# Performance work log

Measured on AMD Instinct MI355X. Metric: run time of the kernel, lower is better.

Reference implementation:

```python
import jax, jax.numpy as jnp
import numpy as np

D_MODEL, N_HEAD, D_FF = 768, 12, 3072
HEAD_DIM = D_MODEL // N_HEAD
EPS = 1e-5


def _layernorm(x, g, b):
    mu = jnp.mean(x, axis=-1, keepdims=True)
    var = jnp.mean((x - mu) ** 2, axis=-1, keepdims=True)
    return (x - mu) * jax.lax.rsqrt(var + EPS) * g + b


def setup_inputs() -> dict:
    key = jax.random.key(0)
    ks = jax.random.split(key, 14)
    s = 1.0 / np.sqrt(D_MODEL)
    sf = 1.0 / np.sqrt(D_FF)
    inp = {
        "x": jax.random.normal(ks[0], (2, 2048, D_MODEL), dtype=jnp.float32),
        "Wq": jax.random.normal(ks[1], (D_MODEL, D_MODEL), dtype=jnp.float32) * s,
        "bq": jnp.zeros((D_MODEL,), jnp.float32),
        "Wk": jax.random.normal(ks[2], (D_MODEL, D_MODEL), dtype=jnp.float32) * s,
        "bk": jnp.zeros((D_MODEL,), jnp.float32),
        "Wv": jax.random.normal(ks[3], (D_MODEL, D_MODEL), dtype=jnp.float32) * s,
        "bv": jnp.zeros((D_MODEL,), jnp.float32),
        "Wo": jax.random.normal(ks[4], (D_MODEL, D_MODEL), dtype=jnp.float32) * s,
        "bo": jnp.zeros((D_MODEL,), jnp.float32),
        "W1": jax.random.normal(ks[5], (D_MODEL, D_FF), dtype=jnp.float32) * s,
        "b1": jnp.zeros((D_FF,), jnp.float32),
        "W2": jax.random.normal(ks[6], (D_FF, D_MODEL), dtype=jnp.float32) * sf,
        "b2": jnp.zeros((D_MODEL,), jnp.float32),
        "ln1_g": jnp.ones((D_MODEL,), jnp.float32),
        "ln1_b": jnp.zeros((D_MODEL,), jnp.float32),
        "ln2_g": jnp.ones((D_MODEL,), jnp.float32),
        "ln2_b": jnp.zeros((D_MODEL,), jnp.float32),
    }
    return inp


def reference(x, Wq, bq, Wk, bk, Wv, bv, Wo, bo, W1, b1, W2, b2,
              ln1_g, ln1_b, ln2_g, ln2_b):
    B, S, D = x.shape
    # projections -> [B, H, S, hd]
    def proj(W, b):
        return (x @ W + b).reshape(B, S, N_HEAD, HEAD_DIM).transpose(0, 2, 1, 3)
    q, k, v = proj(Wq, bq), proj(Wk, bk), proj(Wv, bv)
    scores = jnp.einsum("bhqd,bhkd->bhqk", q, k) / jnp.sqrt(
        jnp.asarray(HEAD_DIM, jnp.float32))
    attn = jax.nn.softmax(scores, axis=-1)
    ctx = jnp.einsum("bhqk,bhkd->bhqd", attn, v)
    ctx = ctx.transpose(0, 2, 1, 3).reshape(B, S, D)
    attn_out = ctx @ Wo + bo
    h = _layernorm(x + attn_out, ln1_g, ln1_b)
    ffn = jax.nn.gelu(h @ W1 + b1, approximate=False) @ W2 + b2
    return _layernorm(h + ffn, ln2_g, ln2_b)
```

## Files before the change

kernel.cpp:

```cpp
#include <hip/hip_runtime.h>
#include <hip/hip_bf16.h>
#include <cstdint>
#include <cstddef>

typedef unsigned short u16;
typedef __bf16 bf16x8 __attribute__((ext_vector_type(8)));
typedef float f32x4 __attribute__((ext_vector_type(4)));

#define MFMA_BF16(a, b, c) __builtin_amdgcn_mfma_f32_16x16x32_bf16((a), (b), (c), 0, 0, 0)

#define GLDS16(g, l)                                                        \
  __builtin_amdgcn_global_load_lds(                                         \
      (__attribute__((address_space(1))) void*)(void*)(g),                  \
      (__attribute__((address_space(3))) void*)(void*)(l), 16, 0, 0)

#define QSCALE 0.18033688011112042f
#define PSTRIDE ((size_t)4096 * 768)

__device__ __forceinline__ u16 f2bf(float x) {
  union { float f; unsigned u; } c; c.f = x;
  unsigned u = c.u;
  unsigned r = (u + 0x7fffu + ((u >> 16) & 1u)) >> 16;
  return (u16)r;
}


__global__ __launch_bounds__(256) void transpose_bf16_k(
    const float* __restrict__ in, u16* __restrict__ out, int K, int N) {
  __shared__ float tile[32][33];
  const int tx = threadIdx.x & 31, ty = threadIdx.x >> 5;
  const int bx = blockIdx.x * 32;
  const int by = blockIdx.y * 32;
#pragma unroll
  for (int j = 0; j < 32; j += 8)
    tile[ty + j][tx] = in[(size_t)(by + ty + j) * N + bx + tx];
  __syncthreads();
#pragma unroll
  for (int j = 0; j < 32; j += 8)
    out[(size_t)(bx + ty + j) * K + by + tx] = f2bf(tile[tx][ty + j]);
}

__global__ __launch_bounds__(256) void cvt_bf16_k(
    const float* __restrict__ in, u16* __restrict__ out, int n) {
  int i = (blockIdx.x * 256 + threadIdx.x) * 4;
  if (i + 3 < n) {
    const float4 v = *(const float4*)(in + i);
    ushort4 o;
    o.x = f2bf(v.x); o.y = f2bf(v.y); o.z = f2bf(v.z); o.w = f2bf(v.w);
    *(ushort4*)(out + i) = o;
  }
}

__global__ __launch_bounds__(256) void concat3_k(
    const float* __restrict__ a, const float* __restrict__ b,
    const float* __restrict__ c, float* __restrict__ out) {
  int i = blockIdx.x * 256 + threadIdx.x;
  if (i < 768) out[i] = a[i];
  else if (i < 1536) out[i] = b[i - 768];
  else if (i < 2304) out[i] = c[i - 1536];
}

template <int EPI>
__global__ __launch_bounds__(256) void gemm_bt(
    const u16* __restrict__ A, const u16* __restrict__ BT,
    const float* __restrict__ bias, int M, int N, int K, int kchunk,
    float* __restrict__ outf, u16* __restrict__ outb,
    u16* __restrict__ qo, u16* __restrict__ ko, u16* __restrict__ vto) {
  __shared__ __align__(16) u16 lsA[128 * 64];
  __shared__ __align__(16) u16 lsB[128 * 64];
  const int tid = threadIdx.x;
  const int w = tid >> 6, lane = tid & 63;
  const int wm = w & 1, wn = w >> 1;
  const int lrow = lane & 15, quad = lane >> 4;
  const int m0 = blockIdx.y * 128, n0 = blockIdx.x * 128;
  const int kbeg = blockIdx.z * kchunk, kend = kbeg + kchunk;

  f32x4 acc[4][4];
#pragma unroll
  for (int i = 0; i < 4; ++i)
#pragma unroll
    for (int j = 0; j < 4; ++j) acc[i][j] = (f32x4){0.f, 0.f, 0.f, 0.f};

  const int off = tid * 16;
  const int srow = off >> 7;
  const int schunk = (off >> 4) & 7;
  const int sxc = schunk ^ (srow & 7);
  const int scol = sxc * 8;

  const int rsw = lrow & 7;

  for (int k0 = kbeg; k0 < kend; k0 += 64) {
    const u16* ga = A + (size_t)(m0 + srow) * K + k0 + scol;
    const u16* gb = BT + (size_t)(n0 + srow) * K + k0 + scol;
#pragma unroll
    for (int c = 0; c < 4; ++c) {
      GLDS16(ga + (size_t)(c * 32) * K, (char*)lsA + c * 4096 + off);
      GLDS16(gb + (size_t)(c * 32) * K, (char*)lsB + c * 4096 + off);
    }
    __syncthreads();
#pragma unroll
    for (int ks = 0; ks < 2; ++ks) {
      const int slot = ((ks * 4 + quad) ^ rsw) * 8;
      bf16x8 af[4], bfr[4];
#pragma unroll
      for (int ms = 0; ms < 4; ++ms)
        af[ms] = *(const bf16x8*)&lsA[(wm * 64 + ms * 16 + lrow) * 64 + slot];
#pragma unroll
      for (int ns = 0; ns < 4; ++ns)
        bfr[ns] = *(const bf16x8*)&lsB[(wn * 64 + ns * 16 + lrow) * 64 + slot];
#pragma unroll
      for (int ms = 0; ms < 4; ++ms)
#pragma unroll
        for (int ns = 0; ns < 4; ++ns)
          acc[ms][ns] = MFMA_BF16(af[ms], bfr[ns], acc[ms][ns]);
    }
    __syncthreads();
  }

  float* const pf = (EPI == 3) ? outf + (size_t)blockIdx.z * M * N : outf;
#pragma unroll
  for (int ms = 0; ms < 4; ++ms) {
    const int rbase = m0 + wm * 64 + ms * 16 + quad * 4;
#pragma unroll
    for (int ns = 0; ns < 4; ++ns) {
      const int col = n0 + wn * 64 + ns * 16 + lrow;
      if constexpr (EPI == 3) {
#pragma unroll
        for (int r = 0; r < 4; ++r)
          pf[(size_t)(rbase + r) * N + col] = acc[ms][ns][r];
      } else if constexpr (EPI == 2) {
        const float bcol = bias[col];
#pragma unroll
        for (int r = 0; r < 4; ++r) {
          float v = acc[ms][ns][r] + bcol;
          float g = 0.5f * v * (1.0f + erff(v * 0.7071067811865476f));
          outb[(size_t)(rbase + r) * N + col] = f2bf(g);
        }
      } else {
        const float bcol = bias[col];
        const int which = col / 768;
        const int rem = col - which * 768;
        const int hh = rem >> 6, dd = rem & 63;
        const int bI = rbase >> 11, sI = rbase & 2047;
        const size_t bh = (size_t)bI * 12 + hh;
        if (which == 0) {
#pragma unroll
          for (int r = 0; r < 4; ++r)
            qo[(bh * 2048 + sI + r) * 64 + dd] = f2bf((acc[ms][ns][r] + bcol) * QSCALE);
        } else if (which == 1) {
#pragma unroll
          for (int r = 0; r < 4; ++r)
            ko[(bh * 2048 + sI + r) * 64 + dd] = f2bf(acc[ms][ns][r] + bcol);
        } else {
          ushort4 pk;
          pk.x = f2bf(acc[ms][ns][0] + bcol);
          pk.y = f2bf(acc[ms][ns][1] + bcol);
          pk.z = f2bf(acc[ms][ns][2] + bcol);
          pk.w = f2bf(acc[ms][ns][3] + bcol);
          *(ushort4*)(vto + (bh * 64 + dd) * 2048 + sI) = pk;
        }
      }
    }
  }
}

__global__ __launch_bounds__(256) void attn_kernel(
    const u16* __restrict__ q, const u16* __restrict__ k,
    const u16* __restrict__ vT, u16* __restrict__ ctx) {
  __shared__ __align__(16) u16 lsK[64 * 64];
  __shared__ __align__(16) u16 lsV[64 * 64];
  __shared__ __align__(16) u16 lsP[4][16 * 64];
  const int tid = threadIdx.x;
  const int w = tid >> 6, lane = tid & 63;
  const int lrow = lane & 15, quad = lane >> 4;
  const int bh = blockIdx.y;
  const int b = bh / 12, h = bh - b * 12;
  const int q0 = blockIdx.x * 64;

  const u16* qbase = q + (size_t)bh * 2048 * 64;
  const u16* kbase = k + (size_t)bh * 2048 * 64;
  const u16* vbase = vT + (size_t)bh * 64 * 2048;

  const int qrow = q0 + w * 16 + lrow;
  const bf16x8 qf0 = *(const bf16x8*)(qbase + (size_t)qrow * 64 + quad * 8);
  const bf16x8 qf1 = *(const bf16x8*)(qbase + (size_t)qrow * 64 + 32 + quad * 8);

  float lsum[4] = {0.f, 0.f, 0.f, 0.f};
  f32x4 oacc[4];
#pragma unroll
  for (int d = 0; d < 4; ++d) oacc[d] = (f32x4){0.f, 0.f, 0.f, 0.f};

  const int off = tid * 16;
  const int srow = off >> 7;
  const int schunk = (off >> 4) & 7;
  const int sxc = schunk ^ (srow & 7);
  const int ksrc = srow * 64 + sxc * 8;
  const int vsrc0 = srow * 2048 + sxc * 8;

  const int c0 = quad ^ (lrow & 7);
  const int rd0 = c0 * 8, rd1 = (c0 ^ 4) * 8;

  u16* const lsPw = &lsP[w][0];
  const int jhi_base = lrow >> 3, jlo = lrow & 7;

  for (int kt = 0; kt < 2048; kt += 64) {
    GLDS16(kbase + (size_t)kt * 64 + ksrc, (char*)lsK + off);
    GLDS16(kbase + (size_t)(kt + 32) * 64 + ksrc, (char*)lsK + 4096 + off);
    GLDS16(vbase + vsrc0 + kt, (char*)lsV + off);
    GLDS16(vbase + vsrc0 + kt + 32 * 2048, (char*)lsV + 4096 + off);
    __syncthreads();

    f32x4 sc[4];
#pragma unroll
    for (int ns = 0; ns < 4; ++ns) {
      sc[ns] = (f32x4){0.f, 0.f, 0.f, 0.f};
      const u16* kr = &lsK[(ns * 16 + lrow) * 64];
      bf16x8 kf0 = *(const bf16x8*)(kr + rd0);
      bf16x8 kf1 = *(const bf16x8*)(kr + rd1);
      sc[ns] = MFMA_BF16(qf0, kf0, sc[ns]);
      sc[ns] = MFMA_BF16(qf1, kf1, sc[ns]);
    }

#pragma unroll
    for (int ns = 0; ns < 4; ++ns) {
      const int jhi = ns * 2 + jhi_base;
#pragma unroll
      for (int r = 0; r < 4; ++r) {
        float p = __builtin_amdgcn_exp2f(sc[ns][r]);
        lsum[r] += p;
        union { float f; unsigned u; } cv; cv.f = p;
        const int m = quad * 4 + r;
        lsPw[m * 64 + ((jhi ^ (m & 7)) * 8) + jlo] = (u16)(cv.u >> 16);
      }
    }

    const u16* pr = lsPw + lrow * 64;
    const bf16x8 pf0 = *(const bf16x8*)(pr + rd0);
    const bf16x8 pf1 = *(const bf16x8*)(pr + rd1);
#pragma unroll
    for (int d = 0; d < 4; ++d) {
      const u16* vr = &lsV[(d * 16 + lrow) * 64];
      bf16x8 vf0 = *(const bf16x8*)(vr + rd0);
      bf16x8 vf1 = *(const bf16x8*)(vr + rd1);
      oacc[d] = MFMA_BF16(pf0, vf0, oacc[d]);
      oacc[d] = MFMA_BF16(pf1, vf1, oacc[d]);
    }
    __syncthreads();
  }

#pragma unroll
  for (int r = 0; r < 4; ++r) {
#pragma unroll
    for (int mm = 1; mm <= 8; mm <<= 1) lsum[r] += __shfl_xor(lsum[r], mm);
  }
  float invl[4];
#pragma unroll
  for (int r = 0; r < 4; ++r) invl[r] = 1.f / lsum[r];

  const int srow_out = q0 + w * 16 + quad * 4;
#pragma unroll
  for (int d = 0; d < 4; ++d)
#pragma unroll
    for (int r = 0; r < 4; ++r)
      ctx[(size_t)(b * 2048 + srow_out + r) * 768 + h * 64 + d * 16 + lrow] =
          f2bf(oacc[d][r] * invl[r]);
}

__global__ __launch_bounds__(256) void ln_kernel(
    const float* __restrict__ parts, int nparts, const float* __restrict__ bias,
    const float* __restrict__ res, const float* __restrict__ g,
    const float* __restrict__ bb, float* __restrict__ outf, u16* __restrict__ outb) {
  const int row = blockIdx.x;
  const int tid = threadIdx.x;
  const float* pr = res + (size_t)row * 768;
  float v[3], s = 0.f, s2 = 0.f;
#pragma unroll
  for (int j = 0; j < 3; ++j) {
    const int c = tid + j * 256;
    float t = bias[c] + pr[c];
    for (int p = 0; p < nparts; ++p)
      t += parts[p * PSTRIDE + (size_t)row * 768 + c];
    v[j] = t; s += t; s2 += t * t;
  }
#pragma unroll
  for (int m = 32; m > 0; m >>= 1) {
    s += __shfl_xor(s, m);
    s2 += __shfl_xor(s2, m);
  }
  __shared__ float red[8];
  const int w = tid >> 6, lane = tid & 63;
  if (lane == 0) { red[w] = s; red[4 + w] = s2; }
  __syncthreads();
  s = red[0] + red[1] + red[2] + red[3];
  s2 = red[4] + red[5] + red[6] + red[7];
  const float mu = s * (1.f / 768.f);
  const float var = s2 * (1.f / 768.f) - mu * mu;
  const float rstd = rsqrtf(var + 1e-5f);
#pragma unroll
  for (int j = 0; j < 3; ++j) {
    const int c = tid + j * 256;
    const float y = (v[j] - mu) * rstd * g[c] + bb[c];
    if (outf) outf[(size_t)row * 768 + c] = y;
    if (outb) outb[(size_t)row * 768 + c] = f2bf(y);
  }
}

extern "C" void kernel_launch(void* const* d_in, const int* in_sizes, int n_in,
                              void* d_out, int out_size, void* d_ws, size_t ws_size,
                              hipStream_t stream) {
  const float* x    = (const float*)d_in[0];
  const float* Wq   = (const float*)d_in[1];
  const float* bq   = (const float*)d_in[2];
  const float* Wk   = (const float*)d_in[3];
  const float* bk   = (const float*)d_in[4];
  const float* Wv   = (const float*)d_in[5];
  const float* bv   = (const float*)d_in[6];
  const float* Wo   = (const float*)d_in[7];
  const float* bo   = (const float*)d_in[8];
  const float* W1   = (const float*)d_in[9];
  const float* b1   = (const float*)d_in[10];
  const float* W2   = (const float*)d_in[11];
  const float* b2   = (const float*)d_in[12];
  const float* ln1g = (const float*)d_in[13];
  const float* ln1b = (const float*)d_in[14];
  const float* ln2g = (const float*)d_in[15];
  const float* ln2b = (const float*)d_in[16];

  char* ws = (char*)d_ws;
  size_t off = 0;
  auto alloc = [&](size_t bytes) {
    void* p = ws + off;
    off += (bytes + 255) & ~(size_t)255;
    return p;
  };
  u16*  WqkvT = (u16*)alloc(2304ull * 768 * 2);
  u16*  WoT   = (u16*)alloc(768ull * 768 * 2);
  u16*  W1T   = (u16*)alloc(3072ull * 768 * 2);
  u16*  W2T   = (u16*)alloc(768ull * 3072 * 2);
  float* bqkv = (float*)alloc(2304 * 4);
  char* bigbase = (char*)alloc(0);
  u16*  xb    = (u16*)alloc(4096ull * 768 * 2);
  u16*  qb    = (u16*)alloc(24ull * 2048 * 64 * 2);
  u16*  kb    = (u16*)alloc(24ull * 2048 * 64 * 2);
  u16*  vtb   = (u16*)alloc(24ull * 64 * 2048 * 2);
  u16*  ctx   = (u16*)alloc(4096ull * 768 * 2);
  float* attno = (float*)alloc(2ull * PSTRIDE * 4);
  float* f2b   = (float*)bigbase;
  float* hbuf  = (float*)alloc(4096ull * 768 * 4);
  u16*  hb    = (u16*)alloc(4096ull * 768 * 2);
  u16*  f1    = (u16*)alloc(4096ull * 3072 * 2);

  transpose_bf16_k<<<dim3(24, 24), 256, 0, stream>>>(Wq, WqkvT, 768, 768);
  transpose_bf16_k<<<dim3(24, 24), 256, 0, stream>>>(Wk, WqkvT + 768 * 768, 768, 768);
  transpose_bf16_k<<<dim3(24, 24), 256, 0, stream>>>(Wv, WqkvT + 2 * 768 * 768, 768, 768);
  transpose_bf16_k<<<dim3(24, 24), 256, 0, stream>>>(Wo, WoT, 768, 768);
  transpose_bf16_k<<<dim3(96, 24), 256, 0, stream>>>(W1, W1T, 768, 3072);
  transpose_bf16_k<<<dim3(24, 96), 256, 0, stream>>>(W2, W2T, 3072, 768);
  concat3_k<<<9, 256, 0, stream>>>(bq, bk, bv, bqkv);
  cvt_bf16_k<<<3072, 256, 0, stream>>>(x, xb, 4096 * 768);

  gemm_bt<0><<<dim3(18, 32, 1), 256, 0, stream>>>(xb, WqkvT, bqkv, 4096, 2304, 768, 768,
                                                  nullptr, nullptr, qb, kb, vtb);
  attn_kernel<<<dim3(32, 24), 256, 0, stream>>>(qb, kb, vtb, ctx);
  gemm_bt<3><<<dim3(6, 32, 2), 256, 0, stream>>>(ctx, WoT, nullptr, 4096, 768, 768, 384,
                                                 attno, nullptr, nullptr, nullptr, nullptr);
  ln_kernel<<<4096, 256, 0, stream>>>(attno, 2, bo, x, ln1g, ln1b, hbuf, hb);
  gemm_bt<2><<<dim3(24, 32, 1), 256, 0, stream>>>(hb, W1T, b1, 4096, 3072, 768, 768,
                                                  nullptr, f1, nullptr, nullptr, nullptr);
  gemm_bt<3><<<dim3(6, 32, 4), 256, 0, stream>>>(f1, W2T, nullptr, 4096, 768, 3072, 768,
                                                 f2b, nullptr, nullptr, nullptr, nullptr);
  ln_kernel<<<4096, 256, 0, stream>>>(f2b, 4, b2, hbuf, ln2g, ln2b, (float*)d_out, nullptr);
}
```

Measured before the change: 312.2 us.

## Split attention over two KV halves with double-buffered LDS and a combine kernel

```diff
diff --git a/kernel.cpp b/kernel.cpp
--- a/kernel.cpp
+++ b/kernel.cpp
@@ -166,9 +166,10 @@
 
 __global__ __launch_bounds__(256) void attn_kernel(
     const u16* __restrict__ q, const u16* __restrict__ k,
-    const u16* __restrict__ vT, u16* __restrict__ ctx) {
-  __shared__ __align__(16) u16 lsK[64 * 64];
-  __shared__ __align__(16) u16 lsV[64 * 64];
+    const u16* __restrict__ vT, u16* __restrict__ opart,
+    float* __restrict__ lpart) {
+  __shared__ __align__(16) u16 lsK[2 * 64 * 64];
+  __shared__ __align__(16) u16 lsV[2 * 64 * 64];
   __shared__ __align__(16) u16 lsP[4][16 * 64];
   const int tid = threadIdx.x;
   const int w = tid >> 6, lane = tid & 63;
@@ -176,6 +177,8 @@
   const int bh = blockIdx.y;
   const int b = bh / 12, h = bh - b * 12;
   const int q0 = blockIdx.x * 64;
+  const int z = blockIdx.z;
+  const int kvbeg = z * 1024;
 
   const u16* qbase = q + (size_t)bh * 2048 * 64;
   const u16* kbase = k + (size_t)bh * 2048 * 64;
@@ -203,18 +206,27 @@
   u16* const lsPw = &lsP[w][0];
   const int jhi_base = lrow >> 3, jlo = lrow & 7;
 
-  for (int kt = 0; kt < 2048; kt += 64) {
-    GLDS16(kbase + (size_t)kt * 64 + ksrc, (char*)lsK + off);
-    GLDS16(kbase + (size_t)(kt + 32) * 64 + ksrc, (char*)lsK + 4096 + off);
-    GLDS16(vbase + vsrc0 + kt, (char*)lsV + off);
-    GLDS16(vbase + vsrc0 + kt + 32 * 2048, (char*)lsV + 4096 + off);
+  auto stage = [&](int kt, int buf) {
+    char* dk = (char*)(lsK + buf * 4096);
+    char* dv = (char*)(lsV + buf * 4096);
+    GLDS16(kbase + (size_t)kt * 64 + ksrc, dk + off);
+    GLDS16(kbase + (size_t)(kt + 32) * 64 + ksrc, dk + 4096 + off);
+    GLDS16(vbase + vsrc0 + kt, dv + off);
+    GLDS16(vbase + vsrc0 + kt + 32 * 2048, dv + 4096 + off);
+  };
+
+  stage(kvbeg, 0);
+  for (int t = 0; t < 16; ++t) {
     __syncthreads();
+    if (t < 15) stage(kvbeg + (t + 1) * 64, (t + 1) & 1);
+    const u16* Kb = lsK + (t & 1) * 4096;
+    const u16* Vb = lsV + (t & 1) * 4096;
 
     f32x4 sc[4];
 #pragma unroll
     for (int ns = 0; ns < 4; ++ns) {
       sc[ns] = (f32x4){0.f, 0.f, 0.f, 0.f};
-      const u16* kr = &lsK[(ns * 16 + lrow) * 64];
+      const u16* kr = Kb + (ns * 16 + lrow) * 64;
       bf16x8 kf0 = *(const bf16x8*)(kr + rd0);
       bf16x8 kf1 = *(const bf16x8*)(kr + rd1);
       sc[ns] = MFMA_BF16(qf0, kf0, sc[ns]);
@@ -239,13 +251,12 @@
     const bf16x8 pf1 = *(const bf16x8*)(pr + rd1);
 #pragma unroll
     for (int d = 0; d < 4; ++d) {
-      const u16* vr = &lsV[(d * 16 + lrow) * 64];
+      const u16* vr = Vb + (d * 16 + lrow) * 64;
       bf16x8 vf0 = *(const bf16x8*)(vr + rd0);
       bf16x8 vf1 = *(const bf16x8*)(vr + rd1);
       oacc[d] = MFMA_BF16(pf0, vf0, oacc[d]);
       oacc[d] = MFMA_BF16(pf1, vf1, oacc[d]);
     }
-    __syncthreads();
   }
 
 #pragma unroll
@@ -253,17 +264,39 @@
 #pragma unroll
     for (int mm = 1; mm <= 8; mm <<= 1) lsum[r] += __shfl_xor(lsum[r], mm);
   }
-  float invl[4];
-#pragma unroll
-  for (int r = 0; r < 4; ++r) invl[r] = 1.f / lsum[r];
 
   const int srow_out = q0 + w * 16 + quad * 4;
+  u16* const op = opart + (size_t)z * PSTRIDE;
 #pragma unroll
   for (int d = 0; d < 4; ++d)
 #pragma unroll
     for (int r = 0; r < 4; ++r)
-      ctx[(size_t)(b * 2048 + srow_out + r) * 768 + h * 64 + d * 16 + lrow] =
-          f2bf(oacc[d][r] * invl[r]);
+      op[(size_t)(b * 2048 + srow_out + r) * 768 + h * 64 + d * 16 + lrow] =
+          f2bf(oacc[d][r]);
+  if (lrow == 0) {
+#pragma unroll
+    for (int r = 0; r < 4; ++r)
+      lpart[(size_t)(z * 24 + bh) * 2048 + srow_out + r] = lsum[r];
+  }
+}
+
+__global__ __launch_bounds__(256) void attn_combine_k(
+    const u16* __restrict__ op, const float* __restrict__ lp,
+    u16* __restrict__ ctx) {
+  const int row = blockIdx.x;
+  const int b = row >> 11, s = row & 2047;
+  const int tid = threadIdx.x;
+#pragma unroll
+  for (int j = 0; j < 3; ++j) {
+    const int c = tid + j * 256;
+    const int h = c >> 6;
+    const size_t li = (size_t)(b * 12 + h) * 2048 + s;
+    const float l = lp[li] + lp[(size_t)24 * 2048 + li];
+    union { unsigned u; float f; } a0, a1;
+    a0.u = (unsigned)op[(size_t)row * 768 + c] << 16;
+    a1.u = (unsigned)op[PSTRIDE + (size_t)row * 768 + c] << 16;
+    ctx[(size_t)row * 768 + c] = f2bf((a0.f + a1.f) / l);
+  }
 }
 
 __global__ __launch_bounds__(256) void ln_kernel(
@@ -346,6 +379,8 @@
   u16*  ctx   = (u16*)alloc(4096ull * 768 * 2);
   float* attno = (float*)alloc(2ull * PSTRIDE * 4);
   float* f2b   = (float*)bigbase;
+  u16*   opart = (u16*)attno;
+  float* lpart = (float*)((char*)attno + 2 * PSTRIDE * 2);
   float* hbuf  = (float*)alloc(4096ull * 768 * 4);
   u16*  hb    = (u16*)alloc(4096ull * 768 * 2);
   u16*  f1    = (u16*)alloc(4096ull * 3072 * 2);
@@ -361,7 +396,8 @@
 
   gemm_bt<0><<<dim3(18, 32, 1), 256, 0, stream>>>(xb, WqkvT, bqkv, 4096, 2304, 768, 768,
                                                   nullptr, nullptr, qb, kb, vtb);
-  attn_kernel<<<dim3(32, 24), 256, 0, stream>>>(qb, kb, vtb, ctx);
+  attn_kernel<<<dim3(32, 24, 2), 256, 0, stream>>>(qb, kb, vtb, opart, lpart);
+  attn_combine_k<<<4096, 256, 0, stream>>>(opart, lpart, ctx);
   gemm_bt<3><<<dim3(6, 32, 2), 256, 0, stream>>>(ctx, WoT, nullptr, 4096, 768, 768, 384,
                                                  attno, nullptr, nullptr, nullptr, nullptr);
   ln_kernel<<<4096, 256, 0, stream>>>(attno, 2, bo, x, ln1g, ln1b, hbuf, hb);
```

Result: slower. 326.6 us (+4.6%).
